# Optimization experiments

Measured on AMD Instinct MI355X. Metric: run time of the kernel, lower is better.

Reference implementation:

```python
import jax, jax.numpy as jnp
import numpy as np

N, L, D, W = 64, 514, 768, 256   # batch, padded token len (incl CLS/SEP), bert dim, max words
H1, H2 = 500, 300                # linear1 out, out_size
LN_EPS = 1e-5


def setup_inputs() -> dict:
    key = jax.random.key(0)
    ks = jax.random.split(key, 6)
    texts = jax.random.normal(ks[0], (N, L, D), dtype=jnp.float32)
    # contiguous ragged spans: lengths in {1,2}, cumulative ends <= 512 = L-2 always
    lens = jax.random.randint(ks[1], (N, W), 1, 3)
    word_ends = jnp.cumsum(lens, axis=1).astype(jnp.int32)
    word_starts = (word_ends - lens).astype(jnp.int32)
    word_length = jax.random.randint(ks[2], (N,), W // 2, W + 1).astype(jnp.int32)
    W1 = jax.random.normal(ks[3], (D, H1), dtype=jnp.float32) * np.float32(1.0 / np.sqrt(D))
    b1 = jnp.zeros((H1,), jnp.float32)
    W2 = jax.random.normal(ks[4], (H1, H2), dtype=jnp.float32) * np.float32(1.0 / np.sqrt(H1))
    b2 = jnp.zeros((H2,), jnp.float32)
    gamma = jnp.ones((H2,), jnp.float32)
    beta = jnp.zeros((H2,), jnp.float32)
    return dict(texts=texts, word_starts=word_starts, word_ends=word_ends,
                word_length=word_length, W1=W1, b1=b1, W2=W2, b2=b2,
                gamma=gamma, beta=beta)


def reference(texts, word_starts, word_ends, word_length, W1, b1, W2, b2, gamma, beta):
    # texts: (N, L, D) BERT output; drop [CLS]/[SEP]
    tok = texts[:, 1:-1, :]  # (N, L-2, D)
    # offset-based segment mean: prefix sums over token axis
    csum = jnp.concatenate([jnp.zeros_like(tok[:, :1]), jnp.cumsum(tok, axis=1)], axis=1)  # (N, L-1, D)
    e = word_ends[:, :, None].astype(jnp.int32)
    s = word_starts[:, :, None].astype(jnp.int32)
    seg_sum = jnp.take_along_axis(csum, e, axis=1) - jnp.take_along_axis(csum, s, axis=1)  # (N, W, D)
    cnt = (word_ends - word_starts).astype(texts.dtype)[:, :, None]
    pooled = seg_sum / jnp.maximum(cnt, 1.0)
    # pad_sequence semantics: words beyond word_length[i] are zero
    mask = (jnp.arange(W)[None, :] < word_length[:, None])[:, :, None]
    pooled = jnp.where(mask, pooled, jnp.zeros((), texts.dtype))
    # MLP + LayerNorm: norm(relu(linear2(relu(linear1(x)))))
    h = jax.nn.relu(pooled @ W1 + b1)
    h = jax.nn.relu(h @ W2 + b2)
    mu = jnp.mean(h, axis=-1, keepdims=True)
    var = jnp.mean(jnp.square(h - mu), axis=-1, keepdims=True)
    return (h - mu) * jax.lax.rsqrt(var + LN_EPS) * gamma + beta  # (N, W, 300)
```

## Files before the change

### kernel.cpp

```cpp
#include <hip/hip_runtime.h>
#include <hip/hip_bf16.h>


#define N_  64
#define L_  514
#define D_  768
#define W_  256
#define H1_ 500
#define H1P 512
#define H2_ 300
#define H2P 320
#define LN_EPS 1e-5f
#define M_  (N_ * W_)

typedef __bf16 bf16x8 __attribute__((ext_vector_type(8)));
typedef float  f32x4  __attribute__((ext_vector_type(4)));

__device__ __forceinline__ void load_lds16(const void* g, void* l) {
    __builtin_amdgcn_global_load_lds(
        (const __attribute__((address_space(1))) void*)g,
        (__attribute__((address_space(3))) void*)l, 16, 0, 0);
}

__device__ __forceinline__ uint2 pack4(f32x4 v) {
    union { __hip_bfloat16 h[4]; uint2 u; } o;
    o.h[0] = __float2bfloat16(v[0]); o.h[1] = __float2bfloat16(v[1]);
    o.h[2] = __float2bfloat16(v[2]); o.h[3] = __float2bfloat16(v[3]);
    return o.u;
}

#define POOL_B (M_ / 4)
#define CW1_B  (24 * 16)
#define CW2_B  (16 * 10)

__global__ __launch_bounds__(256) void prep_kernel(
    const float* __restrict__ texts, const int* __restrict__ wstart,
    const int* __restrict__ wend, const int* __restrict__ wlen,
    const float* __restrict__ W1, const float* __restrict__ W2,
    __hip_bfloat16* __restrict__ pooled, __hip_bfloat16* __restrict__ W1T,
    __hip_bfloat16* __restrict__ W2T)
{
    __shared__ float tile[32][33];
    int b = blockIdx.x;
    if (b < POOL_B) {
        const int wave = threadIdx.x >> 6, lane = threadIdx.x & 63;
        const int idx = b * 4 + wave;
        const int n = idx >> 8, w = idx & (W_ - 1);
        const int s = wstart[idx], e = wend[idx];
        const bool live = (w < wlen[n]);
        const float inv = live ? 1.0f / (float)max(e - s, 1) : 0.f;
        f32x4 a0 = {}, a1 = {}, a2 = {};
        if (live) {
            const float* base = texts + ((size_t)n * L_ + 1 + s) * D_ + lane * 4;
            for (int r = 0; r < e - s; ++r) {
                const float* p = base + (size_t)r * D_;
                a0 += *(const f32x4*)(p);
                a1 += *(const f32x4*)(p + 256);
                a2 += *(const f32x4*)(p + 512);
            }
            a0 *= inv; a1 *= inv; a2 *= inv;
        }
        __hip_bfloat16* dst = pooled + (size_t)idx * D_ + lane * 4;
        *(uint2*)(dst)       = pack4(a0);
        *(uint2*)(dst + 256) = pack4(a1);
        *(uint2*)(dst + 512) = pack4(a2);
    } else if (b < POOL_B + CW1_B) {
        int t = b - POOL_B;
        int kt = t % 24, nt = t / 24;
        int r = threadIdx.x >> 5, c = threadIdx.x & 31;
        #pragma unroll
        for (int i = 0; i < 4; ++i) {
            int kk = kt * 32 + r + i * 8;
            int nn = nt * 32 + c;
            tile[r + i * 8][c] = (nn < H1_) ? W1[(size_t)kk * H1_ + nn] : 0.f;
        }
        __syncthreads();
        #pragma unroll
        for (int i = 0; i < 4; ++i) {
            int nn = nt * 32 + r + i * 8;
            int kk = kt * 32 + c;
            W1T[(size_t)nn * D_ + kk] = __float2bfloat16(tile[c][r + i * 8]);
        }
    } else {
        int t = b - POOL_B - CW1_B;
        int kt = t % 16, nt = t / 16;
        int r = threadIdx.x >> 5, c = threadIdx.x & 31;
        #pragma unroll
        for (int i = 0; i < 4; ++i) {
            int kk = kt * 32 + r + i * 8;
            int nn = nt * 32 + c;
            tile[r + i * 8][c] =
                (nn < H2_ && kk < H1_) ? W2[(size_t)kk * H2_ + nn] : 0.f;
        }
        __syncthreads();
        #pragma unroll
        for (int i = 0; i < 4; ++i) {
            int nn = nt * 32 + r + i * 8;
            int kk = kt * 32 + c;
            W2T[(size_t)nn * H1P + kk] = __float2bfloat16(tile[c][r + i * 8]);
        }
    }
}

__global__ __launch_bounds__(512, 1) void gemm1_kernel(
    const ushort* __restrict__ A, const ushort* __restrict__ B,
    const float* __restrict__ b1, ushort* __restrict__ h1)
{
    constexpr int BUFB = 49152;
    __shared__ __align__(16) char bufs[3 * BUFB];
    const int tid  = threadIdx.x;
    const int wave = tid >> 6, lane = tid & 63;
    const int wm = wave >> 1, wn = wave & 1;
    const int t256 = (blockIdx.x & 7) * 32 + (blockIdx.x >> 3);
    const int bm = (t256 >> 2) * 256, bn = (t256 & 3) * 128;
    const int lrow8 = lane >> 3, lslot8 = lane & 7;
    const int g = lane >> 4, fr = lane & 15;

    f32x4 acc[4][4] = {};

    auto stage = [&](int buf, int kt) {
        char* base = bufs + buf * BUFB;
        #pragma unroll
        for (int c0 = 0; c0 < 6; ++c0) {
            int c = wave + c0 * 8;
            int row; const ushort* src;
            if (c < 32) { row = c * 8 + lrow8;        src = A + (size_t)(bm + row) * D_; }
            else        { row = (c - 32) * 8 + lrow8; src = B + (size_t)(bn + row) * D_; }
            int sslot = lslot8 ^ (row & 7);
            load_lds16(src + kt + sslot * 8, base + c * 1024);
        }
    };

    auto compute = [&](int t) {
        const char* base = bufs + (t % 3) * BUFB;
        #pragma unroll
        for (int h = 0; h < 2; ++h) {
            bf16x8 af[4], bf[4];
            #pragma unroll
            for (int mi = 0; mi < 4; ++mi) {
                int r = wm * 64 + mi * 16 + fr;
                af[mi] = *(const bf16x8*)(base + r * 128 + ((((h << 2) + g) ^ (r & 7)) << 4));
            }
            #pragma unroll
            for (int ni = 0; ni < 4; ++ni) {
                int r = wn * 64 + ni * 16 + fr;
                bf[ni] = *(const bf16x8*)(base + 32768 + r * 128 + ((((h << 2) + g) ^ (r & 7)) << 4));
            }
            __builtin_amdgcn_s_setprio(1);
            #pragma unroll
            for (int mi = 0; mi < 4; ++mi)
                #pragma unroll
                for (int ni = 0; ni < 4; ++ni)
                    acc[mi][ni] = __builtin_amdgcn_mfma_f32_16x16x32_bf16(
                        af[mi], bf[ni], acc[mi][ni], 0, 0, 0);
            __builtin_amdgcn_s_setprio(0);
        }
    };

    stage(0, 0); stage(1, 64);
    for (int t = 0; t < 11; ++t) {
        asm volatile("s_waitcnt vmcnt(6)" ::: "memory");
        __builtin_amdgcn_s_barrier();
        if (t + 2 < 12) stage((t + 2) % 3, (t + 2) * 64);
        compute(t);
    }
    asm volatile("s_waitcnt vmcnt(0)" ::: "memory");
    __builtin_amdgcn_s_barrier();
    compute(11);

    #pragma unroll
    for (int mi = 0; mi < 4; ++mi)
        #pragma unroll
        for (int ni = 0; ni < 4; ++ni) {
            int col = bn + wn * 64 + ni * 16 + fr;
            float bv = (col < H1_) ? b1[col] : 0.f;
            #pragma unroll
            for (int j = 0; j < 4; ++j) {
                int row = bm + wm * 64 + mi * 16 + g * 4 + j;
                float v = acc[mi][ni][j] + bv;
                ((__hip_bfloat16*)h1)[(size_t)row * H1P + col] =
                    __float2bfloat16(v > 0.f ? v : 0.f);
            }
        }
}

__global__ __launch_bounds__(512, 1) void gemm2_ln_kernel(
    const ushort* __restrict__ A, const ushort* __restrict__ B,
    const float* __restrict__ b2, const float* __restrict__ gamma,
    const float* __restrict__ beta, float* __restrict__ out)
{
    constexpr int BUFB = 24576;
    __shared__ __align__(16) char bufs[4 * BUFB];
    __shared__ float red[2][32][4][2];
    const int tid  = threadIdx.x;
    const int wave = tid >> 6, lane = tid & 63;
    const int wm = wave >> 2, wn = wave & 3;
    const int bm = blockIdx.x * 64;
    const int lrow = lane >> 2, lslot = lane & 3;
    const int g = lane >> 4, fr = lane & 15;

    f32x4 acc[2][5] = {};

    auto stage = [&](int buf, int kt) {
        char* base = bufs + buf * BUFB;
        #pragma unroll
        for (int c0 = 0; c0 < 3; ++c0) {
            int c = wave + c0 * 8;
            int row; const ushort* src;
            if (c < 4) { row = c * 16 + lrow; src = A + (size_t)(bm + row) * H1P; }
            else       { row = (c - 4) * 16 + lrow; src = B + (size_t)row * H1P; }
            int sslot = lslot ^ ((row >> 1) & 3);
            load_lds16(src + kt + sslot * 8, base + c * 1024);
        }
    };

    auto compute = [&](int t) {
        const char* base = bufs + (t & 3) * BUFB;
        bf16x8 af[2], bf[5];
        #pragma unroll
        for (int mi = 0; mi < 2; ++mi) {
            int r = wm * 32 + mi * 16 + fr;
            af[mi] = *(const bf16x8*)(base + r * 64 + ((g ^ ((r >> 1) & 3)) << 4));
        }
        #pragma unroll
        for (int ni = 0; ni < 5; ++ni) {
            int r = wn * 80 + ni * 16 + fr;
            bf[ni] = *(const bf16x8*)(base + 4096 + r * 64 + ((g ^ ((r >> 1) & 3)) << 4));
        }
        __builtin_amdgcn_s_setprio(1);
        #pragma unroll
        for (int mi = 0; mi < 2; ++mi)
            #pragma unroll
            for (int ni = 0; ni < 5; ++ni)
                acc[mi][ni] = __builtin_amdgcn_mfma_f32_16x16x32_bf16(
                    af[mi], bf[ni], acc[mi][ni], 0, 0, 0);
        __builtin_amdgcn_s_setprio(0);
    };

    stage(0, 0); stage(1, 32); stage(2, 64);
    for (int t = 0; t < 14; ++t) {
        asm volatile("s_waitcnt vmcnt(6)" ::: "memory");
        __builtin_amdgcn_s_barrier();
        if (t + 3 < 16) stage((t + 3) & 3, (t + 3) * 32);
        compute(t);
    }
    asm volatile("s_waitcnt vmcnt(3)" ::: "memory");
    __builtin_amdgcn_s_barrier();
    compute(14);
    asm volatile("s_waitcnt vmcnt(0)" ::: "memory");
    __builtin_amdgcn_s_barrier();
    compute(15);

    float vals[2][5][4];
    float rsum[2][4] = {}, rsq[2][4] = {};
    #pragma unroll
    for (int ni = 0; ni < 5; ++ni) {
        int col = wn * 80 + ni * 16 + fr;
        float bv = (col < H2_) ? b2[col] : 0.f;
        #pragma unroll
        for (int mi = 0; mi < 2; ++mi)
            #pragma unroll
            for (int j = 0; j < 4; ++j) {
                float v = acc[mi][ni][j] + bv;
                v = v > 0.f ? v : 0.f;
                vals[mi][ni][j] = v;
                rsum[mi][j] += v;
                rsq[mi][j]  += v * v;
            }
    }
    #pragma unroll
    for (int off = 1; off < 16; off <<= 1)
        #pragma unroll
        for (int mi = 0; mi < 2; ++mi)
            #pragma unroll
            for (int j = 0; j < 4; ++j) {
                rsum[mi][j] += __shfl_xor(rsum[mi][j], off);
                rsq[mi][j]  += __shfl_xor(rsq[mi][j], off);
            }
    if (fr == 0) {
        #pragma unroll
        for (int mi = 0; mi < 2; ++mi)
            #pragma unroll
            for (int j = 0; j < 4; ++j) {
                int r32 = mi * 16 + g * 4 + j;
                red[wm][r32][wn][0] = rsum[mi][j];
                red[wm][r32][wn][1] = rsq[mi][j];
            }
    }
    __syncthreads();
    #pragma unroll
    for (int mi = 0; mi < 2; ++mi) {
        #pragma unroll
        for (int j = 0; j < 4; ++j) {
            int r32 = mi * 16 + g * 4 + j;
            float S  = red[wm][r32][0][0] + red[wm][r32][1][0]
                     + red[wm][r32][2][0] + red[wm][r32][3][0];
            float SQ = red[wm][r32][0][1] + red[wm][r32][1][1]
                     + red[wm][r32][2][1] + red[wm][r32][3][1];
            float mu   = S * (1.0f / H2_);
            float var  = SQ * (1.0f / H2_) - mu * mu;
            float rstd = rsqrtf(var + LN_EPS);
            int row = bm + wm * 32 + r32;
            #pragma unroll
            for (int ni = 0; ni < 5; ++ni) {
                int col = wn * 80 + ni * 16 + fr;
                if (col < H2_)
                    out[(size_t)row * H2_ + col] =
                        (vals[mi][ni][j] - mu) * rstd * gamma[col] + beta[col];
            }
        }
    }
}

extern "C" void kernel_launch(void* const* d_in, const int* in_sizes, int n_in,
                              void* d_out, int out_size, void* d_ws, size_t ws_size,
                              hipStream_t stream)
{
    const float* texts  = (const float*)d_in[0];
    const int*   wstart = (const int*)  d_in[1];
    const int*   wend   = (const int*)  d_in[2];
    const int*   wlen   = (const int*)  d_in[3];
    const float* W1     = (const float*)d_in[4];
    const float* b1     = (const float*)d_in[5];
    const float* W2     = (const float*)d_in[6];
    const float* b2     = (const float*)d_in[7];
    const float* gamma  = (const float*)d_in[8];
    const float* beta   = (const float*)d_in[9];
    float* out = (float*)d_out;

    ushort* pooled = (ushort*)d_ws;
    ushort* h1     = pooled + (size_t)M_ * D_;
    ushort* W1T    = h1 + (size_t)M_ * H1P;
    ushort* W2T    = W1T + (size_t)H1P * D_;

    prep_kernel<<<POOL_B + CW1_B + CW2_B, 256, 0, stream>>>(
        texts, wstart, wend, wlen, W1, W2,
        (__hip_bfloat16*)pooled, (__hip_bfloat16*)W1T, (__hip_bfloat16*)W2T);

    gemm1_kernel<<<256, 512, 0, stream>>>(pooled, W1T, b1, h1);

    gemm2_ln_kernel<<<M_ / 64, 512, 0, stream>>>(h1, W2T, b2, gamma, beta, out);
}
```

Measured before the change: 55.16 us.

## Stage GEMM1 epilogue through LDS and swizzle block-to-XCD mapping

The GEMM1 epilogue now writes bf16 results into per-wave LDS tiles and then stores them to global memory as 16-byte vectors, replacing scattered 2-byte stores. The pooling blocks and the gemm2 blocks get their block indices remapped so that neighbouring work lands on the same XCD, which is meant to improve L2 locality. This adds an extra barrier and an LDS round trip, and it relies on the staging buffers being free after the last compute step.

```diff
diff --git a/kernel.cpp b/kernel.cpp
--- a/kernel.cpp
+++ b/kernel.cpp
@@ -43,16 +43,18 @@
     __shared__ float tile[32][33];
     int b = blockIdx.x;
     if (b < POOL_B) {
-        const int wave = threadIdx.x >> 6, lane = threadIdx.x & 63;
-        const int idx = b * 4 + wave;
+        const int e = b & 7, u = b >> 3;
+        const int q = e * 8 + (u & 7);
+        const int idx = (q * 64 + (u >> 3)) * 4 + (threadIdx.x >> 6);
+        const int lane = threadIdx.x & 63;
         const int n = idx >> 8, w = idx & (W_ - 1);
-        const int s = wstart[idx], e = wend[idx];
+        const int s = wstart[idx], ee = wend[idx];
         const bool live = (w < wlen[n]);
-        const float inv = live ? 1.0f / (float)max(e - s, 1) : 0.f;
+        const float inv = live ? 1.0f / (float)max(ee - s, 1) : 0.f;
         f32x4 a0 = {}, a1 = {}, a2 = {};
         if (live) {
             const float* base = texts + ((size_t)n * L_ + 1 + s) * D_ + lane * 4;
-            for (int r = 0; r < e - s; ++r) {
+            for (int r = 0; r < ee - s; ++r) {
                 const float* p = base + (size_t)r * D_;
                 a0 += *(const f32x4*)(p);
                 a1 += *(const f32x4*)(p + 256);
@@ -167,21 +169,36 @@
     asm volatile("s_waitcnt vmcnt(0)" ::: "memory");
     __builtin_amdgcn_s_barrier();
     compute(11);
-
-    #pragma unroll
-    for (int mi = 0; mi < 4; ++mi)
-        #pragma unroll
-        for (int ni = 0; ni < 4; ++ni) {
-            int col = bn + wn * 64 + ni * 16 + fr;
-            float bv = (col < H1_) ? b1[col] : 0.f;
-            #pragma unroll
-            for (int j = 0; j < 4; ++j) {
-                int row = bm + wm * 64 + mi * 16 + g * 4 + j;
-                float v = acc[mi][ni][j] + bv;
-                ((__hip_bfloat16*)h1)[(size_t)row * H1P + col] =
-                    __float2bfloat16(v > 0.f ? v : 0.f);
-            }
-        }
+    __builtin_amdgcn_s_barrier();
+
+    {
+        char* wb = bufs + wave * 8704;
+        #pragma unroll
+        for (int mi = 0; mi < 4; ++mi)
+            #pragma unroll
+            for (int ni = 0; ni < 4; ++ni) {
+                int col = bn + wn * 64 + ni * 16 + fr;
+                float bv = (col < H1_) ? b1[col] : 0.f;
+                #pragma unroll
+                for (int j = 0; j < 4; ++j) {
+                    float v = acc[mi][ni][j] + bv;
+                    int lr = mi * 16 + g * 4 + j;
+                    int lc = ni * 16 + fr;
+                    *(ushort*)(wb + lr * 136 + lc * 2) =
+                        __hip_bfloat16_raw(__float2bfloat16(v > 0.f ? v : 0.f)).x;
+                }
+            }
+        __builtin_amdgcn_s_barrier();
+        #pragma unroll
+        for (int i = 0; i < 8; ++i) {
+            int lr = i * 8 + (lane >> 3);
+            int c8 = lane & 7;
+            uint4 v = *(const uint4*)(wb + lr * 136 + c8 * 16);
+            int row = bm + wm * 64 + lr;
+            int col = bn + wn * 64 + c8 * 8;
+            *(uint4*)((__hip_bfloat16*)h1 + (size_t)row * H1P + col) = v;
+        }
+    }
 }
 
 __global__ __launch_bounds__(512, 1) void gemm2_ln_kernel(
@@ -195,7 +212,8 @@
     const int tid  = threadIdx.x;
     const int wave = tid >> 6, lane = tid & 63;
     const int wm = wave >> 2, wn = wave & 3;
-    const int bm = blockIdx.x * 64;
+    const int bswz = (blockIdx.x & 7) * 32 + (blockIdx.x >> 3);
+    const int bm = bswz * 64;
     const int lrow = lane >> 2, lslot = lane & 3;
     const int g = lane >> 4, fr = lane & 15;
 
```

Result: no change. 55.82 us (+1.2%).
